# Performance work log

Measured on AMD Instinct MI355X. Metric: run time of the kernel, lower is better.

The kernel has to match this reference:

```python
import jax, jax.numpy as jnp
import numpy as np

# Dimensions: B batch, I genes per case, E embed dim, V sga vocab, NH heads,
# NB attention blocks, CAN cancer types, OUT output genes
B, I, E, V, NH, NB, CAN, OUT = 128, 800, 512, 19000, 8, 4, 10, 5000
MASK_VAL = -1e9


def setup_inputs() -> dict:
    key = jax.random.key(0)
    ks = jax.random.split(key, 10)
    s = 0.02
    sga = jax.random.randint(ks[0], (B, I), 0, V)            # 0 == padding
    can = jax.random.randint(ks[1], (B,), 0, CAN)
    emb_tables = jax.random.normal(ks[2], (NB, V + 1, E), jnp.float32) * s
    emb_tables = emb_tables.at[:, 0, :].set(0.0)              # padding_idx=0
    Wk = jax.random.normal(ks[3], (NB, E, E), jnp.float32) * s   # transform2Keys
    bk = jnp.zeros((NB, E), jnp.float32)
    Wq = jax.random.normal(ks[4], (NB, E, NH), jnp.float32) * s  # queryKeyMatch
    bq = jnp.zeros((NB, NH), jnp.float32)
    can_emb = jax.random.normal(ks[5], (CAN, E), jnp.float32) * s
    Wh = jax.random.normal(ks[6], (NB - 1, E, E), jnp.float32) * s  # residual linears (no bias)
    Wfinal = jax.random.normal(ks[7], (E, OUT), jnp.float32) * s    # final linear (no bias)
    return dict(sga=sga, can=can, emb_tables=emb_tables, Wk=Wk, bk=bk,
                Wq=Wq, bq=bq, can_emb=can_emb, Wh=Wh, Wfinal=Wfinal)


def _sga_block(sga, table, Wk_b, bk_b, Wq_b, bq_b):
    embs = table[sga]                                   # [B,I,E] gather
    keys = jnp.tanh(embs @ Wk_b + bk_b)                 # [B,I,E]
    scores = keys @ Wq_b + bq_b                         # [B,I,NH]
    scores = jnp.where(sga[..., None] == 0, MASK_VAL, scores)
    A = jax.nn.softmax(scores, axis=1)                  # softmax over genes I
    emb = jnp.einsum('bin,bie->be', A, embs)            # sum over heads + genes
    attn_wt = A.sum(axis=2)                             # [B,I]
    return emb, attn_wt


def reference(sga, can, emb_tables, Wk, bk, Wq, bq, can_emb, Wh, Wfinal):
    emb0, attn0 = _sga_block(sga, emb_tables[0], Wk[0], bk[0], Wq[0], bq[0])
    curr = jax.nn.relu(emb0 + can_emb[can])             # using_cancer_type=True
    attns = [attn0]
    hiddens = [curr]
    for i in range(1, NB):
        emb_i, attn_i = _sga_block(sga, emb_tables[i], Wk[i], bk[i], Wq[i], bq[i])
        curr = emb_i + curr @ Wh[i - 1]
        curr = jax.nn.relu(curr) if i < NB - 1 else jax.nn.sigmoid(curr)
        attns.append(attn_i)
        hiddens.append(curr)
    preds = curr @ Wfinal                               # [B,OUT]
    return preds, jnp.stack(attns), jnp.stack(hiddens)
```

## Files before the change

### kernel.cpp

```cpp
#include <hip/hip_runtime.h>
#include <hip/hip_bf16.h>

constexpr int Bn   = 128;
constexpr int In   = 800;
constexpr int En   = 512;
constexpr int V1   = 19001;
constexpr int NHn  = 8;
constexpr int NBn  = 4;
constexpr int OUTn = 5000;

constexpr int OFF_ATTN = Bn * OUTn;
constexpr int OFF_HID  = OFF_ATTN + NBn * Bn * In;

typedef __attribute__((ext_vector_type(8))) short bf16x8;
typedef __attribute__((ext_vector_type(8))) unsigned short u16x8;
typedef __attribute__((ext_vector_type(4))) float f32x4;

__device__ inline ushort f2bf(float x) {
    __hip_bfloat16 h = __float2bfloat16(x);
    return *reinterpret_cast<ushort*>(&h);
}
__device__ inline float bf2f(ushort u) {
    return __uint_as_float(((unsigned)u) << 16);
}
__device__ inline void gl_lds16(const ushort* g, ushort* l) {
    __builtin_amdgcn_global_load_lds(
        (const __attribute__((address_space(1))) void*)g,
        (__attribute__((address_space(3))) void*)l, 16, 0, 0);
}

__device__ inline float fast_tanh(float x) {
    const float e = __expf(2.0f * x);
    return 1.0f - 2.0f / (e + 1.0f);
}

#define DPP_XOR1(x) __int_as_float(__builtin_amdgcn_update_dpp( \
    0, __float_as_int(x), 0xB1, 0xF, 0xF, false))
#define DPP_XOR2(x) __int_as_float(__builtin_amdgcn_update_dpp( \
    0, __float_as_int(x), 0x4E, 0xF, 0xF, false))

__global__ __launch_bounds__(256)
void k_prep(const float* __restrict__ Wk, ushort* __restrict__ Wkt) {
    __shared__ float ts[64][65];
    const int n0 = blockIdx.x * 64, k0 = blockIdx.y * 64, nb = blockIdx.z;
    const int t = threadIdx.x;
    {
        const int kr = t >> 2, nc = (t & 3) * 16;
        const float* p = Wk + (((size_t)nb * En) + (k0 + kr)) * En + n0 + nc;
#pragma unroll
        for (int j = 0; j < 4; ++j) {
            const float4 v = *(const float4*)(p + j * 4);
            ts[kr][nc + j * 4 + 0] = v.x; ts[kr][nc + j * 4 + 1] = v.y;
            ts[kr][nc + j * 4 + 2] = v.z; ts[kr][nc + j * 4 + 3] = v.w;
        }
    }
    __syncthreads();
    {
        const int nr = t >> 2, kc = (t & 3) * 16;
        ushort* d = Wkt + (((size_t)nb * En) + (n0 + nr)) * En + k0 + kc;
        ushort4 o;
#pragma unroll
        for (int j = 0; j < 4; ++j) {
            o.x = f2bf(ts[kc + j * 4 + 0][nr]); o.y = f2bf(ts[kc + j * 4 + 1][nr]);
            o.z = f2bf(ts[kc + j * 4 + 2][nr]); o.w = f2bf(ts[kc + j * 4 + 3][nr]);
            *(ushort4*)(d + j * 4) = o;
        }
    }
}

__global__ __launch_bounds__(256)
void k_cvt(const float* __restrict__ T, ushort* __restrict__ Tbf,
           const long long n8) {
    const long long stride = (long long)gridDim.x * 256;
    for (long long i = (long long)blockIdx.x * 256 + threadIdx.x; i < n8;
         i += stride) {
        const float4 f0 = *(const float4*)(T + i * 8);
        const float4 f1 = *(const float4*)(T + i * 8 + 4);
        u16x8 o;
        o[0] = f2bf(f0.x); o[1] = f2bf(f0.y); o[2] = f2bf(f0.z); o[3] = f2bf(f0.w);
        o[4] = f2bf(f1.x); o[5] = f2bf(f1.y); o[6] = f2bf(f1.z); o[7] = f2bf(f1.w);
        *(u16x8*)(Tbf + i * 8) = o;
    }
}

__global__ __launch_bounds__(256, 2)
void k_scores_fast(const ushort* __restrict__ Tbf, const ushort* __restrict__ Wkt,
                   const float* __restrict__ bk, const float* __restrict__ Wq,
                   float* __restrict__ scoresv) {
    __shared__ ushort Bs[2][512][32];
    __shared__ union { ushort A[2][64][32]; float red[4][64][NHn]; } u;

    const int mblk = blockIdx.x, nb = blockIdx.y;
    const int v0 = mblk * 64;
    const int tid = threadIdx.x, lane = tid & 63, w = tid >> 6;
    const int q = lane >> 4, c = lane & 15;
    const int gsw = (q ^ (c & 3)) * 8;

    const ushort* Ab = Tbf + (size_t)nb * V1 * En;
    const ushort* Wn = Wkt + (size_t)nb * En * En;

    const int ar  = w * 16 + (lane >> 2);
    const int ag  = (lane & 3) ^ ((lane >> 2) & 3);
    const int vrow = min(v0 + ar, V1 - 1);
    const ushort* agp = Ab + (size_t)vrow * En + ag * 8;

    f32x4 acc[4][8];
#pragma unroll
    for (int mt = 0; mt < 4; ++mt)
#pragma unroll
        for (int nt = 0; nt < 8; ++nt) acc[mt][nt] = (f32x4)0.0f;

    auto stageB = [&](int buf, int k0) {
#pragma unroll
        for (int j = 0; j < 8; ++j) {
            const int nrow = (w * 8 + j) * 16;
            const int r = nrow + (lane >> 2);
            const int gf = (lane & 3) ^ ((lane >> 2) & 3);
            const ushort* gp = Wn + (size_t)r * En + k0 + gf * 8;
            gl_lds16(gp, &Bs[buf][nrow][0]);
        }
    };
    auto stageA = [&](int buf, int k0) {
        gl_lds16(agp + k0, &u.A[buf][w * 16][0]);
    };

    stageA(0, 0);
    stageB(0, 0);
    __syncthreads();

    for (int it = 0; it < 16; ++it) {
        const int cur = it & 1, nxt = cur ^ 1;
        if (it < 15) {
            const int k0n = (it + 1) * 32;
            stageA(nxt, k0n);
            stageB(nxt, k0n);
        }
        bf16x8 aF[4], bF[8];
#pragma unroll
        for (int mt = 0; mt < 4; ++mt)
            aF[mt] = *(bf16x8*)&u.A[cur][mt * 16 + c][gsw];
#pragma unroll
        for (int nt = 0; nt < 8; ++nt)
            bF[nt] = *(bf16x8*)&Bs[cur][w * 128 + nt * 16 + c][gsw];
#pragma unroll
        for (int nt = 0; nt < 8; ++nt)
#pragma unroll
            for (int mt = 0; mt < 4; ++mt)
                acc[mt][nt] = __builtin_amdgcn_mfma_f32_16x16x32_bf16(
                    aF[mt], bF[nt], acc[mt][nt], 0, 0, 0);
        __syncthreads();
    }

#pragma unroll
    for (int nt = 0; nt < 8; ++nt) {
        const int col = w * 128 + nt * 16 + c;
        const float bkv = bk[nb * En + col];
#pragma unroll
        for (int mt = 0; mt < 4; ++mt)
#pragma unroll
            for (int r = 0; r < 4; ++r)
                acc[mt][nt][r] = fast_tanh(acc[mt][nt][r] + bkv);
    }

    for (int h = 0; h < NHn; ++h) {
        float wqh[8];
#pragma unroll
        for (int nt = 0; nt < 8; ++nt) {
            const int col = w * 128 + nt * 16 + c;
            wqh[nt] = Wq[((size_t)nb * En + col) * NHn + h];
        }
        float p[4][4];
#pragma unroll
        for (int mt = 0; mt < 4; ++mt)
#pragma unroll
            for (int r = 0; r < 4; ++r) {
                float s = 0.f;
#pragma unroll
                for (int nt = 0; nt < 8; ++nt) s += acc[mt][nt][r] * wqh[nt];
                s += DPP_XOR1(s);
                s += DPP_XOR2(s);
                s += __shfl_xor(s, 4, 64);
                s += __shfl_xor(s, 8, 64);
                p[mt][r] = s;
            }
        if (c == h) {
#pragma unroll
            for (int mt = 0; mt < 4; ++mt)
#pragma unroll
                for (int r = 0; r < 4; ++r)
                    u.red[w][mt * 16 + q * 4 + r][h] = p[mt][r];
        }
    }
    __syncthreads();

    for (int idx = tid; idx < 64 * NHn; idx += 256) {
        const int row = idx >> 3, h = idx & 7;
        const int vr = v0 + row;
        if (vr < V1)
            scoresv[((size_t)nb * V1 + vr) * NHn + h] =
                u.red[0][row][h] + u.red[1][row][h] +
                u.red[2][row][h] + u.red[3][row][h];
    }
}

__global__ __launch_bounds__(256, 2)
void k_scores_slow(const float* __restrict__ T, const ushort* __restrict__ Wkt,
                   const float* __restrict__ bk, const float* __restrict__ Wq,
                   float* __restrict__ scoresv) {
    __shared__ ushort Bs[2][512][32];
    __shared__ union { ushort A[2][64][32]; float red[4][64][NHn]; } u;

    const int mblk = blockIdx.x, nb = blockIdx.y;
    const int v0 = mblk * 64;
    const int tid = threadIdx.x, lane = tid & 63, w = tid >> 6;
    const int q = lane >> 4, c = lane & 15;
    const int gsw = (q ^ (c & 3)) * 8;

    const float*  Tb = T + (size_t)nb * V1 * En;
    const ushort* Wn = Wkt + (size_t)nb * En * En;

    const int arow = tid >> 2, akq = tid & 3;
    const int aswz = (akq ^ (arow & 3)) * 8;
    const int vra = v0 + arow;
    const float* agp = Tb + (size_t)vra * En + akq * 8;

    f32x4 acc[4][8];
#pragma unroll
    for (int mt = 0; mt < 4; ++mt)
#pragma unroll
        for (int nt = 0; nt < 8; ++nt) acc[mt][nt] = (f32x4)0.0f;

    auto stageB = [&](int buf, int k0) {
#pragma unroll
        for (int j = 0; j < 8; ++j) {
            const int nrow = (w * 8 + j) * 16;
            const int r = nrow + (lane >> 2);
            const int gf = (lane & 3) ^ ((lane >> 2) & 3);
            const ushort* gp = Wn + (size_t)r * En + k0 + gf * 8;
            gl_lds16(gp, &Bs[buf][nrow][0]);
        }
    };
    auto loadA = [&](int k0, float4& f0, float4& f1) {
        if (vra < V1) {
            f0 = *(const float4*)(agp + k0);
            f1 = *(const float4*)(agp + k0 + 4);
        } else {
            f0 = make_float4(0.f, 0.f, 0.f, 0.f);
            f1 = f0;
        }
    };
    auto writeA = [&](int buf, float4 f0, float4 f1) {
        u16x8 o;
        o[0] = f2bf(f0.x); o[1] = f2bf(f0.y); o[2] = f2bf(f0.z); o[3] = f2bf(f0.w);
        o[4] = f2bf(f1.x); o[5] = f2bf(f1.y); o[6] = f2bf(f1.z); o[7] = f2bf(f1.w);
        *(u16x8*)&u.A[buf][arow][aswz] = o;
    };

    stageB(0, 0);
    {
        float4 f0, f1;
        loadA(0, f0, f1);
        writeA(0, f0, f1);
    }
    __syncthreads();

    for (int it = 0; it < 16; ++it) {
        const int cur = it & 1, nxt = cur ^ 1;
        const int k0n = (it + 1) * 32;
        float4 p0, p1;
        if (it < 15) {
            stageB(nxt, k0n);
            loadA(k0n, p0, p1);
        }
        bf16x8 aF[4], bF[8];
#pragma unroll
        for (int mt = 0; mt < 4; ++mt)
            aF[mt] = *(bf16x8*)&u.A[cur][mt * 16 + c][gsw];
#pragma unroll
        for (int nt = 0; nt < 8; ++nt)
            bF[nt] = *(bf16x8*)&Bs[cur][w * 128 + nt * 16 + c][gsw];
#pragma unroll
        for (int nt = 0; nt < 8; ++nt)
#pragma unroll
            for (int mt = 0; mt < 4; ++mt)
                acc[mt][nt] = __builtin_amdgcn_mfma_f32_16x16x32_bf16(
                    aF[mt], bF[nt], acc[mt][nt], 0, 0, 0);
        if (it < 15) writeA(nxt, p0, p1);
        __syncthreads();
    }

#pragma unroll
    for (int nt = 0; nt < 8; ++nt) {
        const int col = w * 128 + nt * 16 + c;
        const float bkv = bk[nb * En + col];
#pragma unroll
        for (int mt = 0; mt < 4; ++mt)
#pragma unroll
            for (int r = 0; r < 4; ++r)
                acc[mt][nt][r] = fast_tanh(acc[mt][nt][r] + bkv);
    }

    for (int h = 0; h < NHn; ++h) {
        float wqh[8];
#pragma unroll
        for (int nt = 0; nt < 8; ++nt) {
            const int col = w * 128 + nt * 16 + c;
            wqh[nt] = Wq[((size_t)nb * En + col) * NHn + h];
        }
        float p[4][4];
#pragma unroll
        for (int mt = 0; mt < 4; ++mt)
#pragma unroll
            for (int r = 0; r < 4; ++r) {
                float s = 0.f;
#pragma unroll
                for (int nt = 0; nt < 8; ++nt) s += acc[mt][nt][r] * wqh[nt];
                s += DPP_XOR1(s);
                s += DPP_XOR2(s);
                s += __shfl_xor(s, 4, 64);
                s += __shfl_xor(s, 8, 64);
                p[mt][r] = s;
            }
        if (c == h) {
#pragma unroll
            for (int mt = 0; mt < 4; ++mt)
#pragma unroll
                for (int r = 0; r < 4; ++r)
                    u.red[w][mt * 16 + q * 4 + r][h] = p[mt][r];
        }
    }
    __syncthreads();

    for (int idx = tid; idx < 64 * NHn; idx += 256) {
        const int row = idx >> 3, h = idx & 7;
        const int vr = v0 + row;
        if (vr < V1)
            scoresv[((size_t)nb * V1 + vr) * NHn + h] =
                u.red[0][row][h] + u.red[1][row][h] +
                u.red[2][row][h] + u.red[3][row][h];
    }
}

__global__ __launch_bounds__(256)
void k_softmax(const int* __restrict__ sga, const float* __restrict__ scoresv,
               float* __restrict__ attn_out) {
    const int b  = blockIdx.x;
    const int nb = blockIdx.y;
    const int tid = threadIdx.x;
    const int lane = tid & 63;
    const int wid  = tid >> 6;
    __shared__ float red[4 * NHn];

    float sc[4][NHn];
    int ivals[4];
#pragma unroll
    for (int s = 0; s < 4; ++s) {
        const int i = tid + s * 256;
        ivals[s] = i;
        if (i < In) {
            const int v = sga[b * In + i];
            const float4 s0 = *(const float4*)(scoresv + ((size_t)nb * V1 + v) * NHn);
            const float4 s1 = *(const float4*)(scoresv + ((size_t)nb * V1 + v) * NHn + 4);
            sc[s][0] = s0.x; sc[s][1] = s0.y; sc[s][2] = s0.z; sc[s][3] = s0.w;
            sc[s][4] = s1.x; sc[s][5] = s1.y; sc[s][6] = s1.z; sc[s][7] = s1.w;
            if (v == 0) {
#pragma unroll
                for (int n = 0; n < NHn; ++n) sc[s][n] = -1e9f;
            }
        } else {
#pragma unroll
            for (int n = 0; n < NHn; ++n) sc[s][n] = -3.0e38f;
        }
    }

    float lm[NHn];
#pragma unroll
    for (int n = 0; n < NHn; ++n)
        lm[n] = fmaxf(fmaxf(sc[0][n], sc[1][n]), fmaxf(sc[2][n], sc[3][n]));
#pragma unroll
    for (int m = 1; m < 64; m <<= 1) {
#pragma unroll
        for (int n = 0; n < NHn; ++n) lm[n] = fmaxf(lm[n], __shfl_xor(lm[n], m, 64));
    }
    if (lane == 0) {
#pragma unroll
        for (int n = 0; n < NHn; ++n) red[wid * NHn + n] = lm[n];
    }
    __syncthreads();
    float M[NHn];
#pragma unroll
    for (int n = 0; n < NHn; ++n)
        M[n] = fmaxf(fmaxf(red[n], red[NHn + n]), fmaxf(red[2 * NHn + n], red[3 * NHn + n]));
    __syncthreads();

    float ls[NHn];
#pragma unroll
    for (int n = 0; n < NHn; ++n) ls[n] = 0.f;
#pragma unroll
    for (int s = 0; s < 4; ++s) {
#pragma unroll
        for (int n = 0; n < NHn; ++n) {
            sc[s][n] = expf(sc[s][n] - M[n]);
            ls[n] += sc[s][n];
        }
    }
#pragma unroll
    for (int m = 1; m < 64; m <<= 1) {
#pragma unroll
        for (int n = 0; n < NHn; ++n) ls[n] += __shfl_xor(ls[n], m, 64);
    }
    if (lane == 0) {
#pragma unroll
        for (int n = 0; n < NHn; ++n) red[wid * NHn + n] = ls[n];
    }
    __syncthreads();
    float inv[NHn];
#pragma unroll
    for (int n = 0; n < NHn; ++n) {
        const float S = red[n] + red[NHn + n] + red[2 * NHn + n] + red[3 * NHn + n];
        inv[n] = 1.0f / S;
    }

#pragma unroll
    for (int s = 0; s < 4; ++s) {
        if (ivals[s] < In) {
            float w = 0.f;
#pragma unroll
            for (int n = 0; n < NHn; ++n) w += sc[s][n] * inv[n];
            attn_out[((size_t)nb * Bn + b) * In + ivals[s]] = w;
        }
    }
}

template <bool TBF>
__global__ __launch_bounds__(512)
void k_emb(const int* __restrict__ sga, const float* __restrict__ attn,
           const float* __restrict__ T, const ushort* __restrict__ Tbf,
           float* __restrict__ emb) {
    const int b  = blockIdx.x;
    const int nb = blockIdx.y;
    __shared__ int   sv[In];
    __shared__ float sw[In];
    __shared__ float pa[8][En];
    for (int idx = threadIdx.x; idx < In; idx += 512) {
        sv[idx] = sga[b * In + idx];
        sw[idx] = attn[((size_t)nb * Bn + b) * In + idx];
    }
    __syncthreads();
    const int wave = threadIdx.x >> 6, lane = threadIdx.x & 63;
    float a[8];
#pragma unroll
    for (int j = 0; j < 8; ++j) a[j] = 0.f;

    if (TBF) {
        const ushort* Tb = Tbf + (size_t)nb * V1 * En;
#pragma unroll 10
        for (int g = 0; g < 100; ++g) {
            const int i = wave * 100 + g;
            const int v = sv[i];
            const float w = sw[i];
            const u16x8 t = *(const u16x8*)(Tb + (size_t)v * En + lane * 8);
#pragma unroll
            for (int j = 0; j < 8; ++j) a[j] += w * bf2f(t[j]);
        }
    } else {
        const float* Tb = T + (size_t)nb * V1 * En;
#pragma unroll 10
        for (int g = 0; g < 100; ++g) {
            const int i = wave * 100 + g;
            const int v = sv[i];
            const float w = sw[i];
            const float4* p = (const float4*)(Tb + (size_t)v * En) + lane * 2;
            const float4 t0 = p[0], t1 = p[1];
            a[0] += w * t0.x; a[1] += w * t0.y; a[2] += w * t0.z; a[3] += w * t0.w;
            a[4] += w * t1.x; a[5] += w * t1.y; a[6] += w * t1.z; a[7] += w * t1.w;
        }
    }
#pragma unroll
    for (int j = 0; j < 8; ++j) pa[wave][lane * 8 + j] = a[j];
    __syncthreads();
    const int t = threadIdx.x;
    float s = 0.f;
#pragma unroll
    for (int wv = 0; wv < 8; ++wv) s += pa[wv][t];
    emb[((size_t)nb * Bn + b) * En + t] = s;
}

__global__ __launch_bounds__(256)
void k_step0(const float* __restrict__ emb0, const int* __restrict__ can,
             const float* __restrict__ can_emb, float* __restrict__ cur,
             float* __restrict__ hid) {
    const int b = blockIdx.x;
    const int e0 = threadIdx.x * 2;
    const int c = can[b];
    float2 v = *(const float2*)(emb0 + (size_t)b * En + e0);
    const float2 ce = *(const float2*)(can_emb + (size_t)c * En + e0);
    v.x = fmaxf(v.x + ce.x, 0.f);
    v.y = fmaxf(v.y + ce.y, 0.f);
    *(float2*)(cur + (size_t)b * En + e0) = v;
    *(float2*)(hid + (size_t)b * En + e0) = v;
}

__global__ __launch_bounds__(256)
void k_step(const float* __restrict__ embi, const float* __restrict__ prev,
            const float* __restrict__ Whi, float* __restrict__ cur,
            float* __restrict__ hid, const int sig) {
    const int b = blockIdx.x, cc = blockIdx.y;
    __shared__ float pr[En];
    __shared__ float part[2][128];
    pr[threadIdx.x]       = prev[(size_t)b * En + threadIdx.x];
    pr[threadIdx.x + 256] = prev[(size_t)b * En + threadIdx.x + 256];
    __syncthreads();
    const int col = cc * 128 + (threadIdx.x & 127);
    const int kh  = threadIdx.x >> 7;
    float s = 0.f;
    const float* Wp = Whi + (size_t)(kh * 256) * En + col;
#pragma unroll 8
    for (int k = 0; k < 256; ++k) s += pr[kh * 256 + k] * Wp[(size_t)k * En];
    part[kh][threadIdx.x & 127] = s;
    __syncthreads();
    if (threadIdx.x < 128) {
        float a = part[0][threadIdx.x] + part[1][threadIdx.x] +
                  embi[(size_t)b * En + col];
        if (sig) a = 1.0f / (1.0f + expf(-a));
        else     a = fmaxf(a, 0.f);
        cur[(size_t)b * En + col] = a;
        hid[(size_t)b * En + col] = a;
    }
}

__global__ __launch_bounds__(256, 2)
void k_preds(const float* __restrict__ cur, const float* __restrict__ Wf,
             float* __restrict__ preds) {
    __shared__ float cs[32 * En];
    const int nt = blockIdx.x;
    const int bt = blockIdx.y;
    for (int idx = threadIdx.x; idx < 32 * 128; idx += 256) {
        const int row = idx >> 7;
        const int c4  = (idx & 127) << 2;
        *(float4*)(cs + row * En + c4) =
            *(const float4*)(cur + (size_t)(bt * 32 + row) * En + c4);
    }
    __syncthreads();
    const int lane = threadIdx.x & 63;
    const int rgrp = threadIdx.x >> 6;
    const int col = nt * 64 + lane;
    float acc[8];
#pragma unroll
    for (int j = 0; j < 8; ++j) acc[j] = 0.f;
    const bool ok = (col < OUTn);
    for (int k = 0; k < En; k += 4) {
        float w0 = 0.f, w1 = 0.f, w2 = 0.f, w3 = 0.f;
        if (ok) {
            w0 = Wf[(size_t)(k + 0) * OUTn + col];
            w1 = Wf[(size_t)(k + 1) * OUTn + col];
            w2 = Wf[(size_t)(k + 2) * OUTn + col];
            w3 = Wf[(size_t)(k + 3) * OUTn + col];
        }
#pragma unroll
        for (int j = 0; j < 8; ++j) {
            const float4 cv = *(const float4*)(cs + (rgrp * 8 + j) * En + k);
            acc[j] += cv.x * w0 + cv.y * w1 + cv.z * w2 + cv.w * w3;
        }
    }
    if (ok) {
#pragma unroll
        for (int j = 0; j < 8; ++j)
            preds[(size_t)(bt * 32 + rgrp * 8 + j) * OUTn + col] = acc[j];
    }
}

extern "C" void kernel_launch(void* const* d_in, const int* in_sizes, int n_in,
                              void* d_out, int out_size, void* d_ws, size_t ws_size,
                              hipStream_t stream) {
    const int*   sga     = (const int*)d_in[0];
    const int*   can     = (const int*)d_in[1];
    const float* T       = (const float*)d_in[2];
    const float* Wk      = (const float*)d_in[3];
    const float* bk      = (const float*)d_in[4];
    const float* Wq      = (const float*)d_in[5];
    const float* can_emb = (const float*)d_in[7];
    const float* Wh      = (const float*)d_in[8];
    const float* Wf      = (const float*)d_in[9];

    float* out = (float*)d_out;
    float* ws  = (float*)d_ws;

    float* scoresv = ws;
    float* embw    = scoresv + (size_t)NBn * V1 * NHn;
    float* cur0    = embw + (size_t)NBn * Bn * En;
    float* cur1    = cur0 + (size_t)Bn * En;
    ushort* Wkt    = (ushort*)(cur1 + (size_t)Bn * En);
    ushort* Tbf    = Wkt + (size_t)NBn * En * En;
    const size_t need_full =
        (size_t)(scoresv - ws) * 4 +
        ((size_t)NBn * V1 * NHn + (size_t)NBn * Bn * En + 2 * (size_t)Bn * En) * 4 +
        (size_t)NBn * En * En * 2 + (size_t)NBn * V1 * En * 2;
    const bool useTbf = (ws_size >= need_full);

    float* preds_out = out;
    float* attn_out  = out + OFF_ATTN;
    float* hid_out   = out + OFF_HID;

    k_prep<<<dim3(8, 8, NBn), 256, 0, stream>>>(Wk, Wkt);
    if (useTbf) {
        const long long n8 = (long long)NBn * V1 * En / 8;
        k_cvt<<<2048, 256, 0, stream>>>(T, Tbf, n8);
        k_scores_fast<<<dim3((V1 + 63) / 64, NBn), 256, 0, stream>>>(
            Tbf, Wkt, bk, Wq, scoresv);
    } else {
        k_scores_slow<<<dim3((V1 + 63) / 64, NBn), 256, 0, stream>>>(
            T, Wkt, bk, Wq, scoresv);
    }
    k_softmax<<<dim3(Bn, NBn), 256, 0, stream>>>(sga, scoresv, attn_out);
    if (useTbf)
        k_emb<true><<<dim3(Bn, NBn), 512, 0, stream>>>(sga, attn_out, T, Tbf, embw);
    else
        k_emb<false><<<dim3(Bn, NBn), 512, 0, stream>>>(sga, attn_out, T, Tbf, embw);
    k_step0<<<Bn, 256, 0, stream>>>(embw, can, can_emb, cur0, hid_out);
    k_step<<<dim3(Bn, 4), 256, 0, stream>>>(embw + 1 * Bn * En, cur0,
                                            Wh + 0 * En * En, cur1,
                                            hid_out + 1 * (size_t)Bn * En, 0);
    k_step<<<dim3(Bn, 4), 256, 0, stream>>>(embw + 2 * Bn * En, cur1,
                                            Wh + 1 * En * En, cur0,
                                            hid_out + 2 * (size_t)Bn * En, 0);
    k_step<<<dim3(Bn, 4), 256, 0, stream>>>(embw + 3 * Bn * En, cur0,
                                            Wh + 2 * En * En, cur1,
                                            hid_out + 3 * (size_t)Bn * En, 1);
    k_preds<<<dim3((OUTn + 63) / 64, Bn / 32), 256, 0, stream>>>(cur1, Wf, preds_out);
}
```

Measured before the change: 541.7 us.

## Store Wk in k-tile-major layout and transpose Wq for coalesced score-kernel loads

Wk is now pre-transposed into a k-tile-major bf16 layout, so that each 32-wide K slice of the B operand is one contiguous chunk that global_load_lds can stage with coalesced reads. The LDS swizzle in both score kernels changes to match. A new pre-pass transposes Wq so each head's weights are contiguous for the epilogue loads. The tanh divide becomes a hardware reciprocal, and the conversion kernel's grid is doubled. This adds a small extra kernel launch and workspace, and the rcp-based tanh is slightly less precise.

```diff
diff --git a/kernel.cpp b/kernel.cpp
--- a/kernel.cpp
+++ b/kernel.cpp
@@ -31,7 +31,7 @@
 
 __device__ inline float fast_tanh(float x) {
     const float e = __expf(2.0f * x);
-    return 1.0f - 2.0f / (e + 1.0f);
+    return 1.0f - 2.0f * __builtin_amdgcn_rcpf(e + 1.0f);
 }
 
 #define DPP_XOR1(x) __int_as_float(__builtin_amdgcn_update_dpp( \
@@ -57,14 +57,27 @@
     __syncthreads();
     {
         const int nr = t >> 2, kc = (t & 3) * 16;
-        ushort* d = Wkt + (((size_t)nb * En) + (n0 + nr)) * En + k0 + kc;
-        ushort4 o;
+        const int n = n0 + nr;
 #pragma unroll
         for (int j = 0; j < 4; ++j) {
+            const int k = k0 + kc + j * 4;
+            const int kt = k >> 5, ks = k & 31;
+            ushort* d = Wkt + (size_t)nb * En * En + (size_t)kt * En * 32 +
+                        (size_t)n * 32 + ks;
+            ushort4 o;
             o.x = f2bf(ts[kc + j * 4 + 0][nr]); o.y = f2bf(ts[kc + j * 4 + 1][nr]);
             o.z = f2bf(ts[kc + j * 4 + 2][nr]); o.w = f2bf(ts[kc + j * 4 + 3][nr]);
-            *(ushort4*)(d + j * 4) = o;
-        }
+            *(ushort4*)d = o;
+        }
+    }
+}
+
+__global__ __launch_bounds__(256)
+void k_prepq(const float* __restrict__ Wq, float* __restrict__ Wqt) {
+    const int nb = blockIdx.x;
+    for (int idx = threadIdx.x; idx < En * NHn; idx += 256) {
+        const int h = idx >> 9, n = idx & (En - 1);
+        Wqt[(size_t)nb * NHn * En + idx] = Wq[((size_t)nb * En + n) * NHn + h];
     }
 }
 
@@ -85,7 +98,7 @@
 
 __global__ __launch_bounds__(256, 2)
 void k_scores_fast(const ushort* __restrict__ Tbf, const ushort* __restrict__ Wkt,
-                   const float* __restrict__ bk, const float* __restrict__ Wq,
+                   const float* __restrict__ bk, const float* __restrict__ Wqt,
                    float* __restrict__ scoresv) {
     __shared__ ushort Bs[2][512][32];
     __shared__ union { ushort A[2][64][32]; float red[4][64][NHn]; } u;
@@ -94,15 +107,16 @@
     const int v0 = mblk * 64;
     const int tid = threadIdx.x, lane = tid & 63, w = tid >> 6;
     const int q = lane >> 4, c = lane & 15;
-    const int gsw = (q ^ (c & 3)) * 8;
+    const int gsw = (q ^ (c >> 2)) * 8;
 
     const ushort* Ab = Tbf + (size_t)nb * V1 * En;
     const ushort* Wn = Wkt + (size_t)nb * En * En;
 
-    const int ar  = w * 16 + (lane >> 2);
-    const int ag  = (lane & 3) ^ ((lane >> 2) & 3);
+    const int sg = (lane & 3) ^ ((lane >> 4) & 3);
+
+    const int ar   = w * 16 + (lane >> 2);
     const int vrow = min(v0 + ar, V1 - 1);
-    const ushort* agp = Ab + (size_t)vrow * En + ag * 8;
+    const ushort* agp = Ab + (size_t)vrow * En + sg * 8;
 
     f32x4 acc[4][8];
 #pragma unroll
@@ -110,13 +124,12 @@
 #pragma unroll
         for (int nt = 0; nt < 8; ++nt) acc[mt][nt] = (f32x4)0.0f;
 
-    auto stageB = [&](int buf, int k0) {
+    auto stageB = [&](int buf, int kt) {
+        const ushort* Wp = Wn + (size_t)kt * En * 32;
 #pragma unroll
         for (int j = 0; j < 8; ++j) {
             const int nrow = (w * 8 + j) * 16;
-            const int r = nrow + (lane >> 2);
-            const int gf = (lane & 3) ^ ((lane >> 2) & 3);
-            const ushort* gp = Wn + (size_t)r * En + k0 + gf * 8;
+            const ushort* gp = Wp + (size_t)(nrow + (lane >> 2)) * 32 + sg * 8;
             gl_lds16(gp, &Bs[buf][nrow][0]);
         }
     };
@@ -131,9 +144,8 @@
     for (int it = 0; it < 16; ++it) {
         const int cur = it & 1, nxt = cur ^ 1;
         if (it < 15) {
-            const int k0n = (it + 1) * 32;
-            stageA(nxt, k0n);
-            stageB(nxt, k0n);
+            stageA(nxt, (it + 1) * 32);
+            stageB(nxt, it + 1);
         }
         bf16x8 aF[4], bF[8];
 #pragma unroll
@@ -162,12 +174,13 @@
                 acc[mt][nt][r] = fast_tanh(acc[mt][nt][r] + bkv);
     }
 
+    const float* Wqn = Wqt + (size_t)nb * NHn * En;
     for (int h = 0; h < NHn; ++h) {
         float wqh[8];
 #pragma unroll
         for (int nt = 0; nt < 8; ++nt) {
             const int col = w * 128 + nt * 16 + c;
-            wqh[nt] = Wq[((size_t)nb * En + col) * NHn + h];
+            wqh[nt] = Wqn[h * En + col];
         }
         float p[4][4];
 #pragma unroll
@@ -214,13 +227,14 @@
     const int v0 = mblk * 64;
     const int tid = threadIdx.x, lane = tid & 63, w = tid >> 6;
     const int q = lane >> 4, c = lane & 15;
-    const int gsw = (q ^ (c & 3)) * 8;
+    const int gsw = (q ^ (c >> 2)) * 8;
+    const int sg = (lane & 3) ^ ((lane >> 4) & 3);
 
     const float*  Tb = T + (size_t)nb * V1 * En;
     const ushort* Wn = Wkt + (size_t)nb * En * En;
 
     const int arow = tid >> 2, akq = tid & 3;
-    const int aswz = (akq ^ (arow & 3)) * 8;
+    const int aswz = (akq ^ ((arow >> 2) & 3)) * 8;
     const int vra = v0 + arow;
     const float* agp = Tb + (size_t)vra * En + akq * 8;
 
@@ -230,13 +244,12 @@
 #pragma unroll
         for (int nt = 0; nt < 8; ++nt) acc[mt][nt] = (f32x4)0.0f;
 
-    auto stageB = [&](int buf, int k0) {
+    auto stageB = [&](int buf, int kt) {
+        const ushort* Wp = Wn + (size_t)kt * En * 32;
 #pragma unroll
         for (int j = 0; j < 8; ++j) {
             const int nrow = (w * 8 + j) * 16;
-            const int r = nrow + (lane >> 2);
-            const int gf = (lane & 3) ^ ((lane >> 2) & 3);
-            const ushort* gp = Wn + (size_t)r * En + k0 + gf * 8;
+            const ushort* gp = Wp + (size_t)(nrow + (lane >> 2)) * 32 + sg * 8;
             gl_lds16(gp, &Bs[buf][nrow][0]);
         }
     };
@@ -269,7 +282,7 @@
         const int k0n = (it + 1) * 32;
         float4 p0, p1;
         if (it < 15) {
-            stageB(nxt, k0n);
+            stageB(nxt, it + 1);
             loadA(k0n, p0, p1);
         }
         bf16x8 aF[4], bF[8];
@@ -590,11 +603,12 @@
     float* embw    = scoresv + (size_t)NBn * V1 * NHn;
     float* cur0    = embw + (size_t)NBn * Bn * En;
     float* cur1    = cur0 + (size_t)Bn * En;
-    ushort* Wkt    = (ushort*)(cur1 + (size_t)Bn * En);
+    float* wqt     = cur1 + (size_t)Bn * En;
+    ushort* Wkt    = (ushort*)(wqt + (size_t)NBn * NHn * En);
     ushort* Tbf    = Wkt + (size_t)NBn * En * En;
     const size_t need_full =
-        (size_t)(scoresv - ws) * 4 +
-        ((size_t)NBn * V1 * NHn + (size_t)NBn * Bn * En + 2 * (size_t)Bn * En) * 4 +
+        ((size_t)NBn * V1 * NHn + (size_t)NBn * Bn * En + 2 * (size_t)Bn * En +
+         (size_t)NBn * NHn * En) * 4 +
         (size_t)NBn * En * En * 2 + (size_t)NBn * V1 * En * 2;
     const bool useTbf = (ws_size >= need_full);
 
@@ -603,11 +617,12 @@
     float* hid_out   = out + OFF_HID;
 
     k_prep<<<dim3(8, 8, NBn), 256, 0, stream>>>(Wk, Wkt);
+    k_prepq<<<NBn, 256, 0, stream>>>(Wq, wqt);
     if (useTbf) {
         const long long n8 = (long long)NBn * V1 * En / 8;
-        k_cvt<<<2048, 256, 0, stream>>>(T, Tbf, n8);
+        k_cvt<<<4096, 256, 0, stream>>>(T, Tbf, n8);
         k_scores_fast<<<dim3((V1 + 63) / 64, NBn), 256, 0, stream>>>(
-            Tbf, Wkt, bk, Wq, scoresv);
+            Tbf, Wkt, bk, wqt, scoresv);
     } else {
         k_scores_slow<<<dim3((V1 + 63) / 64, NBn), 256, 0, stream>>>(
             T, Wkt, bk, Wq, scoresv);
```

Result: no change. 533.1 us (-1.6%).
